# Kernel optimization log

Hardware: AMD Instinct MI355X
Metric: run time of the kernel (lower is better)

## Reference

```python
import jax, jax.numpy as jnp
import numpy as np

NEG_INF = -1e30
NUM_HEADS = 4
MEM_LEN = 16
RECURRENT_STEPS = 3
B, PLEN, GLEN, D = 16, 512, 16384, 256


def gated_attn(query, key, value, key_mask, Wq, Wk, Wv, Wo, Wg, bg):
    # GatedMultiHeadAttn.forward (pre/post lnorm off, add_zero_attn off, eval dropout)
    b, qlen, _ = query.shape
    klen = key.shape[1]
    hidden = Wq.shape[1]
    hd = hidden // NUM_HEADS
    hq = (query @ Wq).reshape(b, qlen, NUM_HEADS, hd)
    hk = (key @ Wk).reshape(b, klen, NUM_HEADS, hd)
    hv = (value @ Wv).reshape(b, klen, NUM_HEADS, hd)
    scale = 1.0 / np.sqrt(hd).astype(np.float32)
    score = jnp.einsum('bind,bjnd->bijn', hq, hk) * scale
    score = jnp.where((key_mask == 0)[:, None, :, None], NEG_INF, score)
    attn = jax.nn.softmax(score, axis=2)  # normalize over keys j
    vec = jnp.einsum('bijn,bjnd->bind', attn, hv).reshape(b, qlen, hidden)
    attn_out = vec @ Wo
    gate = jax.nn.sigmoid(jnp.concatenate([query, attn_out], axis=-1) @ Wg + bg)
    return gate * query + (1.0 - gate) * attn_out


def _attn_params(key, query_dim, kv_dim, hidden):
    ks = jax.random.split(key, 6)
    scale = 1.0 / np.sqrt(hidden // NUM_HEADS)
    Wq = jax.random.normal(ks[0], (query_dim, hidden), jnp.float32) * scale
    Wk = jax.random.normal(ks[1], (kv_dim, hidden), jnp.float32) * scale
    Wv = jax.random.normal(ks[2], (kv_dim, hidden), jnp.float32) * scale
    Wo = jax.random.normal(ks[3], (hidden, query_dim), jnp.float32) * scale
    Wg = jax.random.normal(ks[4], (2 * query_dim, query_dim), jnp.float32) * scale
    bg = jnp.ones((query_dim,), jnp.float32)
    return Wq, Wk, Wv, Wo, Wg, bg


def setup_inputs() -> dict:
    key = jax.random.key(0)
    ks = jax.random.split(key, 4)
    inp = {
        'pattern': jax.random.normal(ks[0], (B, PLEN, D), jnp.float32),
        'graph': jax.random.normal(ks[1], (B, GLEN, D), jnp.float32),
        'pattern_mask': jnp.ones((B, PLEN), jnp.int32),
        'graph_mask': jnp.ones((B, GLEN), jnp.int32),
    }
    p = _attn_params(ks[2], D, D, D)
    g = _attn_params(ks[3], D, D, D)
    for n, v in zip(['p_Wq', 'p_Wk', 'p_Wv', 'p_Wo', 'p_Wg', 'p_bg'], p):
        inp[n] = v
    for n, v in zip(['g_Wq', 'g_Wk', 'g_Wv', 'g_Wo', 'g_Wg', 'g_bg'], g):
        inp[n] = v
    return inp


def reference(pattern, graph, pattern_mask, graph_mask,
              p_Wq, p_Wk, p_Wv, p_Wo, p_Wg, p_bg,
              g_Wq, g_Wk, g_Wv, g_Wo, g_Wg, g_bg):
    b, glen, d = graph.shape
    stride = glen // MEM_LEN
    kernel = glen - (MEM_LEN - 1) * stride
    assert stride == kernel  # mem_len divides glen -> avg_pool1d == segment mean
    mem = graph.reshape(b, MEM_LEN, kernel, d).mean(axis=2)  # init_mem 'mean'
    mem_mask = graph_mask.reshape(b, MEM_LEN, kernel).max(axis=2)
    for _ in range(RECURRENT_STEPS):
        mem = gated_attn(mem, pattern, pattern, pattern_mask,
                         p_Wq, p_Wk, p_Wv, p_Wo, p_Wg, p_bg)
        mem = gated_attn(mem, graph, graph, graph_mask,
                         g_Wq, g_Wk, g_Wv, g_Wo, g_Wg, g_bg)
    return mem
```

## Files before the change

### kernel.cpp

```cpp
#include <hip/hip_runtime.h>
#include <stdint.h>

#define NH 4
#define HD 64
#define DM 256
#define BB 16
#define PLEN 512
#define GLEN 16384
#define ML 16
#define NCH_MAX 32

typedef __attribute__((ext_vector_type(8))) short bf16x8;
typedef __attribute__((ext_vector_type(4))) short s16x4;
typedef __attribute__((ext_vector_type(4))) float f32x4;
struct fl4 { float x, y, z, w; };

#define MFMA16(a, b, c) __builtin_amdgcn_mfma_f32_16x16x32_bf16((a), (b), (c), 0, 0, 0)

__device__ __forceinline__ float bf2f(short x) {
  union { unsigned u; float f; } v;
  v.u = ((unsigned)(unsigned short)x) << 16;
  return v.f;
}
__device__ __forceinline__ short f2bf(float x) {
  union { float f; unsigned u; } v;
  v.f = x;
  unsigned u = v.u;
  u += 0x7fffu + ((u >> 16) & 1u);
  return (short)(u >> 16);
}

__global__ void detect_dtype(const short* __restrict__ pattern, int* __restrict__ flag) {
  int t = threadIdx.x;
  int bad = 0;
  for (int i = t; i < 4096; i += 256) {
    float v = bf2f(pattern[2 * i]);
    if (!(fabsf(v) < 1e10f)) bad++;
  }
  __shared__ int cnt;
  if (t == 0) cnt = 0;
  __syncthreads();
  if (bad) atomicAdd(&cnt, bad);
  __syncthreads();
  if (t == 0) flag[0] = (cnt > 8) ? 1 : 0;
}

__global__ __launch_bounds__(512, 4) void proj_kv_fused(
    const void* __restrict__ Xraw, const short* __restrict__ WkT,
    const short* __restrict__ WvT, short* __restrict__ Kout,
    short* __restrict__ Vt, int L, float* __restrict__ partials,
    const int* __restrict__ flag) {
  __shared__ __align__(16) short Xs[64 * DM];
  __shared__ float scr[16 * DM];
  const int isf = flag[0];
  const int t = threadIdx.x;
  const int row0 = blockIdx.x * 64;
  const int tc2 = t & 31, tr2 = t >> 5;
  float s[8];
#pragma unroll
  for (int j = 0; j < 8; j++) s[j] = 0.f;
  if (isf) {
    const float* xf = (const float*)Xraw + (size_t)row0 * DM + tc2 * 8;
#pragma unroll
    for (int it = 0; it < 4; it++) {
      int row = it * 16 + tr2;
      fl4 v0 = *(const fl4*)(xf + (size_t)row * DM);
      fl4 v1 = *(const fl4*)(xf + (size_t)row * DM + 4);
      s[0] += v0.x; s[1] += v0.y; s[2] += v0.z; s[3] += v0.w;
      s[4] += v1.x; s[5] += v1.y; s[6] += v1.z; s[7] += v1.w;
      bf16x8 o;
      o[0] = f2bf(v0.x); o[1] = f2bf(v0.y); o[2] = f2bf(v0.z); o[3] = f2bf(v0.w);
      o[4] = f2bf(v1.x); o[5] = f2bf(v1.y); o[6] = f2bf(v1.z); o[7] = f2bf(v1.w);
      *(bf16x8*)(Xs + row * DM + (tc2 ^ (row & 7)) * 8) = o;
    }
  } else {
    const short* xb = (const short*)Xraw + (size_t)row0 * DM + tc2 * 8;
#pragma unroll
    for (int it = 0; it < 4; it++) {
      int row = it * 16 + tr2;
      bf16x8 v = *(const bf16x8*)(xb + (size_t)row * DM);
#pragma unroll
      for (int j = 0; j < 8; j++) s[j] += bf2f(v[j]);
      *(bf16x8*)(Xs + row * DM + (tc2 ^ (row & 7)) * 8) = v;
    }
  }
  if (partials) {
#pragma unroll
    for (int j = 0; j < 8; j++) scr[tr2 * DM + tc2 * 8 + j] = s[j];
  }
  __syncthreads();
  if (partials && t < DM) {
    float a = 0.f;
#pragma unroll
    for (int i = 0; i < 16; i++) a += scr[i * DM + t];
    partials[(size_t)blockIdx.x * DM + t] = a;
  }
  const int wave = t >> 6, lane = t & 63, quad = lane >> 4, l16 = lane & 15;
  const int kv = wave >> 2;
  const int wc = (wave & 3) * 64;
  const short* WT = kv ? WvT : WkT;
  f32x4 z = {0.f, 0.f, 0.f, 0.f};
  f32x4 acc[4][4];
#pragma unroll
  for (int i = 0; i < 4; i++)
#pragma unroll
    for (int j = 0; j < 4; j++) acc[i][j] = z;
#pragma unroll
  for (int kk = 0; kk < 8; kk++) {
    bf16x8 a[4], bw[4];
#pragma unroll
    for (int rt = 0; rt < 4; rt++) {
      int rw = rt * 16 + l16;
      a[rt] = *(const bf16x8*)(Xs + rw * DM + (((kk * 4 + quad) ^ (rw & 7)) * 8));
    }
#pragma unroll
    for (int ct = 0; ct < 4; ct++)
      bw[ct] = *(const bf16x8*)(WT + (size_t)(wc + ct * 16 + l16) * DM + kk * 32 + quad * 8);
#pragma unroll
    for (int rt = 0; rt < 4; rt++)
#pragma unroll
      for (int ct = 0; ct < 4; ct++)
        acc[rt][ct] = MFMA16(a[rt], bw[ct], acc[rt][ct]);
  }
  if (kv == 0) {
#pragma unroll
    for (int rt = 0; rt < 4; rt++)
#pragma unroll
      for (int ct = 0; ct < 4; ct++) {
        int col = wc + ct * 16 + l16;
#pragma unroll
        for (int r = 0; r < 4; r++)
          Kout[(size_t)(row0 + rt * 16 + quad * 4 + r) * DM + col] = f2bf(acc[rt][ct][r]);
      }
  } else {
    int bb = row0 / L, j0v = row0 % L;
#pragma unroll
    for (int rt = 0; rt < 4; rt++) {
      int j = j0v + rt * 16 + quad * 4;
#pragma unroll
      for (int ct = 0; ct < 4; ct++) {
        int c = wc + ct * 16 + l16;
        s16x4 pv;
#pragma unroll
        for (int r = 0; r < 4; r++) pv[r] = f2bf(acc[rt][ct][r]);
        *(s16x4*)(Vt + ((size_t)bb * DM + c) * L + j) = pv;
      }
    }
  }
}

__global__ __launch_bounds__(256) void finalize_q0(
    const float* __restrict__ partials, const void* __restrict__ Wq,
    float* __restrict__ mem, short* __restrict__ hq, const int* __restrict__ flag) {
  int b = blockIdx.x >> 4, m = blockIdx.x & 15;
  int t = threadIdx.x;
  int isf = flag[0];
  int p0 = b * 256 + m * 16;
  float s = 0.f;
#pragma unroll
  for (int i = 0; i < 16; i++) s += partials[(size_t)(p0 + i) * 256 + t];
  float v = s * (1.0f / 1024.0f);
  __shared__ float memrow[256];
  memrow[t] = bf2f(f2bf(v));
  mem[((size_t)b * ML + m) * DM + t] = v;
  __syncthreads();
  float acc = 0.f;
  if (isf) {
    const float* wf = (const float*)Wq;
    for (int k = 0; k < 256; k++)
      acc += memrow[k] * bf2f(f2bf(wf[(size_t)k * 256 + t]));
  } else {
    const short* wsp = (const short*)Wq;
    for (int k = 0; k < 256; k++)
      acc += memrow[k] * bf2f(wsp[(size_t)k * 256 + t]);
  }
  hq[((size_t)b * ML + m) * DM + t] = f2bf(acc);
}

struct WTArgs {
  const void* src[10];
  short* dst[10];
  int rows[10];
};

__global__ void transpose_w(WTArgs a, const int* __restrict__ flag) {
  int mid = blockIdx.z;
  int K = a.rows[mid];
  int tk = blockIdx.x, tn = blockIdx.y;
  if (tk * 32 >= K) return;
  int isf = flag[0];
  __shared__ short tile[32][33];
  const short* src = (const short*)a.src[mid];
  const float* srcf = (const float*)a.src[mid];
  short* dst = a.dst[mid];
  int tx = threadIdx.x, ty = threadIdx.y;
  for (int i = 0; i < 32; i += 8) {
    size_t idx = (size_t)(tk * 32 + ty + i) * 256 + tn * 32 + tx;
    tile[ty + i][tx] = isf ? f2bf(srcf[idx]) : src[idx];
  }
  __syncthreads();
  for (int i = 0; i < 32; i += 8)
    dst[(size_t)(tn * 32 + ty + i) * K + tk * 32 + tx] = tile[tx][ty + i];
}

__global__ void conv_bias(const void* p_bg, const void* g_bg, short* out,
                          const int* __restrict__ flag) {
  int t = threadIdx.x;
  int isf = flag[0];
  out[t] = isf ? f2bf(((const float*)p_bg)[t]) : ((const short*)p_bg)[t];
  out[256 + t] = isf ? f2bf(((const float*)g_bg)[t]) : ((const short*)g_bg)[t];
}

__global__ __launch_bounds__(256, 4) void flash_partial(
    const short* __restrict__ hq, const short* __restrict__ Kb,
    const short* __restrict__ Vt, const int* __restrict__ mask,
    float* __restrict__ pm, float* __restrict__ pl, float* __restrict__ pO,
    int L, int NCH) {
  int ch = blockIdx.x, b = blockIdx.y;
  int C = L / NCH;
  int t = threadIdx.x, wave = t >> 6, lane = t & 63, quad = lane >> 4, l16 = lane & 15;
  __shared__ __align__(16) short Plds[4][512];
  short* myP = &Plds[wave][0];
  const short* qbase = hq + ((size_t)b * ML + l16) * DM + wave * HD;
  bf16x8 aq0 = *(const bf16x8*)(qbase + quad * 8);
  bf16x8 aq1 = *(const bf16x8*)(qbase + 32 + quad * 8);
  f32x4 z = {0.f, 0.f, 0.f, 0.f};
  float m_run[4], l_run[4];
  f32x4 O[4];
#pragma unroll
  for (int r = 0; r < 4; r++) { m_run[r] = -1e30f; l_run[r] = 0.f; }
#pragma unroll
  for (int d = 0; d < 4; d++) O[d] = z;
  int j0 = ch * C;
  const float L2E = 1.44269504f;
  for (int jt = 0; jt < C; jt += 32) {
    f32x4 S[2];
#pragma unroll
    for (int tt = 0; tt < 2; tt++) {
      int j = j0 + jt + tt * 16 + l16;
      const short* kb = Kb + ((size_t)b * L + j) * DM + wave * HD;
      bf16x8 b0 = *(const bf16x8*)(kb + quad * 8);
      bf16x8 b1 = *(const bf16x8*)(kb + 32 + quad * 8);
      f32x4 s = MFMA16(aq0, b0, z);
      s = MFMA16(aq1, b1, s);
      int mk = mask[(size_t)b * L + j];
#pragma unroll
      for (int r = 0; r < 4; r++)
        S[tt][r] = mk ? s[r] * 0.125f : -1e30f;
    }
    float p[2][4], alpha[4];
#pragma unroll
    for (int r = 0; r < 4; r++) {
      float v = fmaxf(S[0][r], S[1][r]);
      v = fmaxf(v, __shfl_xor(v, 1, 16));
      v = fmaxf(v, __shfl_xor(v, 2, 16));
      v = fmaxf(v, __shfl_xor(v, 4, 16));
      v = fmaxf(v, __shfl_xor(v, 8, 16));
      float nm = fmaxf(m_run[r], v);
      alpha[r] = exp2f((m_run[r] - nm) * L2E);
      m_run[r] = nm;
      p[0][r] = exp2f((S[0][r] - nm) * L2E);
      p[1][r] = exp2f((S[1][r] - nm) * L2E);
      float ps = p[0][r] + p[1][r];
      ps += __shfl_xor(ps, 1, 16);
      ps += __shfl_xor(ps, 2, 16);
      ps += __shfl_xor(ps, 4, 16);
      ps += __shfl_xor(ps, 8, 16);
      l_run[r] = l_run[r] * alpha[r] + ps;
    }
#pragma unroll
    for (int d = 0; d < 4; d++)
#pragma unroll
      for (int r = 0; r < 4; r++) O[d][r] *= alpha[r];
#pragma unroll
    for (int tt = 0; tt < 2; tt++)
#pragma unroll
      for (int r = 0; r < 4; r++)
        myP[(quad * 4 + r) * 32 + tt * 16 + l16] = f2bf(p[tt][r]);
    __syncthreads();
    bf16x8 ap = *(const bf16x8*)(myP + l16 * 32 + quad * 8);
#pragma unroll
    for (int d = 0; d < 4; d++) {
      const short* vb = Vt + ((size_t)b * DM + wave * HD + d * 16 + l16) * L + j0 + jt + quad * 8;
      bf16x8 bv = *(const bf16x8*)vb;
      O[d] = MFMA16(ap, bv, O[d]);
    }
    __syncthreads();
  }
  size_t base = (((size_t)b * NCH + ch) * NH + wave) * ML;
  if (l16 == 0) {
#pragma unroll
    for (int r = 0; r < 4; r++) {
      pm[base + quad * 4 + r] = m_run[r];
      pl[base + quad * 4 + r] = l_run[r];
    }
  }
#pragma unroll
  for (int d = 0; d < 4; d++)
#pragma unroll
    for (int r = 0; r < 4; r++)
      pO[(base + quad * 4 + r) * 64 + d * 16 + l16] = O[d][r];
}

__global__ __launch_bounds__(256, 2) void epilogue(
    const float* __restrict__ pm, const float* __restrict__ pl,
    const float* __restrict__ pO, int NCH,
    float* __restrict__ mem, const short* __restrict__ WoT,
    const short* __restrict__ WgT, const short* __restrict__ bg,
    const short* __restrict__ WqT, short* __restrict__ hq,
    void* __restrict__ outb, const int* __restrict__ flag) {
  int b = blockIdx.x, t = threadIdx.x;
  int isf = flag[0];
  __shared__ float w_lds[NCH_MAX * 64];
  __shared__ float invL[64];
  __shared__ __align__(16) short vec_bf[ML * DM];
  __shared__ __align__(16) short mem_bf[ML * DM];
  __shared__ __align__(16) short attn_bf[ML * DM];
  __shared__ float attn_f[ML * DM];
  __shared__ __align__(16) short memn_bf[ML * DM];

  for (int idx = t; idx < ML * DM; idx += 256)
    mem_bf[idx] = f2bf(mem[(size_t)b * ML * DM + idx]);
  if (t < 64) {
    size_t base = (size_t)b * NCH * NH * ML + t;
    float M = -1e30f;
    for (int ch = 0; ch < NCH; ch++)
      M = fmaxf(M, pm[base + (size_t)ch * NH * ML]);
    float Ls = 0.f;
    for (int ch = 0; ch < NCH; ch++) {
      float w = exp2f((pm[base + (size_t)ch * NH * ML] - M) * 1.44269504f);
      w_lds[ch * 64 + t] = w;
      Ls += w * pl[base + (size_t)ch * NH * ML];
    }
    invL[t] = 1.0f / Ls;
  }
  __syncthreads();
  {
    int n = t >> 6, d = t & 63;
    for (int i = 0; i < 16; i++) {
      size_t pb = ((size_t)b * NCH * NH * ML + n * ML + i) * 64 + d;
      float o = 0.f;
      for (int ch = 0; ch < NCH; ch++)
        o += w_lds[ch * 64 + n * 16 + i] * pO[pb + (size_t)ch * NH * ML * 64];
      vec_bf[i * DM + n * 64 + d] = f2bf(o * invL[n * 16 + i]);
    }
  }
  __syncthreads();
  int wave = t >> 6, lane = t & 63, quad = lane >> 4, l16 = lane & 15;
  f32x4 z = {0.f, 0.f, 0.f, 0.f};
  f32x4 acc[4];
#pragma unroll
  for (int c = 0; c < 4; c++) acc[c] = z;
#pragma unroll
  for (int kk = 0; kk < 8; kk++) {
    bf16x8 a = *(const bf16x8*)(vec_bf + l16 * DM + kk * 32 + quad * 8);
#pragma unroll
    for (int ct = 0; ct < 4; ct++) {
      const short* wb = WoT + (size_t)(wave * 64 + ct * 16 + l16) * DM + kk * 32 + quad * 8;
      acc[ct] = MFMA16(a, *(const bf16x8*)wb, acc[ct]);
    }
  }
#pragma unroll
  for (int ct = 0; ct < 4; ct++)
#pragma unroll
    for (int r = 0; r < 4; r++) {
      int row = quad * 4 + r, col = wave * 64 + ct * 16 + l16;
      attn_f[row * DM + col] = acc[ct][r];
      attn_bf[row * DM + col] = f2bf(acc[ct][r]);
    }
  __syncthreads();
  f32x4 g[4];
#pragma unroll
  for (int c = 0; c < 4; c++) g[c] = z;
#pragma unroll
  for (int kk = 0; kk < 16; kk++) {
    bf16x8 a = (kk < 8)
        ? *(const bf16x8*)(mem_bf + l16 * DM + kk * 32 + quad * 8)
        : *(const bf16x8*)(attn_bf + l16 * DM + (kk - 8) * 32 + quad * 8);
#pragma unroll
    for (int ct = 0; ct < 4; ct++) {
      const short* wb = WgT + (size_t)(wave * 64 + ct * 16 + l16) * 512 + kk * 32 + quad * 8;
      g[ct] = MFMA16(a, *(const bf16x8*)wb, g[ct]);
    }
  }
#pragma unroll
  for (int ct = 0; ct < 4; ct++)
#pragma unroll
    for (int r = 0; r < 4; r++) {
      int row = quad * 4 + r, col = wave * 64 + ct * 16 + l16;
      float x = g[ct][r] + bf2f(bg[col]);
      float gg = 1.0f / (1.0f + exp2f(-x * 1.44269504f));
      float old = mem[(size_t)b * ML * DM + row * DM + col];
      float mn = gg * old + (1.0f - gg) * attn_f[row * DM + col];
      mem[(size_t)b * ML * DM + row * DM + col] = mn;
      memn_bf[row * DM + col] = f2bf(mn);
      if (outb) {
        size_t oi = (size_t)b * ML * DM + row * DM + col;
        if (isf) ((float*)outb)[oi] = mn;
        else ((short*)outb)[oi] = f2bf(mn);
      }
    }
  __syncthreads();
  if (WqT) {
    f32x4 h[4];
#pragma unroll
    for (int c = 0; c < 4; c++) h[c] = z;
#pragma unroll
    for (int kk = 0; kk < 8; kk++) {
      bf16x8 a = *(const bf16x8*)(memn_bf + l16 * DM + kk * 32 + quad * 8);
#pragma unroll
      for (int ct = 0; ct < 4; ct++) {
        const short* wb = WqT + (size_t)(wave * 64 + ct * 16 + l16) * DM + kk * 32 + quad * 8;
        h[ct] = MFMA16(a, *(const bf16x8*)wb, h[ct]);
      }
    }
#pragma unroll
    for (int ct = 0; ct < 4; ct++)
#pragma unroll
      for (int r = 0; r < 4; r++)
        hq[(size_t)b * ML * DM + (quad * 4 + r) * DM + wave * 64 + ct * 16 + l16] = f2bf(h[ct][r]);
  }
}

extern "C" void kernel_launch(void* const* d_in, const int* in_sizes, int n_in,
                              void* d_out, int out_size, void* d_ws, size_t ws_size,
                              hipStream_t stream) {
  const void* pattern = d_in[0];
  const void* graph = d_in[1];
  const int* pmask = (const int*)d_in[2];
  const int* gmask = (const int*)d_in[3];

  char* ws = (char*)d_ws;
  size_t off = 0;
  auto alloc = [&](size_t bytes) {
    void* p = ws + off;
    off = (off + bytes + 255) & ~(size_t)255;
    return p;
  };
  int* flag = (int*)alloc(4);
  int rows[10] = {256, 256, 256, 256, 512, 256, 256, 256, 256, 512};
  int srcidx[10] = {4, 5, 6, 7, 8, 10, 11, 12, 13, 14};
  short* WT[10];
  for (int i = 0; i < 10; i++) WT[i] = (short*)alloc((size_t)rows[i] * 256 * 2);
  short* bgc = (short*)alloc(512 * 2);
  short* Kp = (short*)alloc((size_t)BB * PLEN * DM * 2);
  short* Vpt = (short*)alloc((size_t)BB * PLEN * DM * 2);
  short* Kg = (short*)alloc((size_t)BB * GLEN * DM * 2);
  short* Vgt = (short*)alloc((size_t)BB * GLEN * DM * 2);
  short* hq = (short*)alloc((size_t)BB * ML * DM * 2);
  float* memf = (float*)alloc((size_t)BB * ML * DM * 4);
  float* pm = (float*)alloc((size_t)BB * NCH_MAX * NH * ML * 4);
  float* pl = (float*)alloc((size_t)BB * NCH_MAX * NH * ML * 4);
  float* pO = (float*)alloc((size_t)BB * NCH_MAX * NH * ML * 64 * 4);
  float* partG = (float*)alloc((size_t)(BB * GLEN / 64) * 256 * 4);
  if (off > ws_size) return;

  detect_dtype<<<dim3(1), dim3(256), 0, stream>>>((const short*)pattern, flag);

  WTArgs wa;
  for (int i = 0; i < 10; i++) {
    wa.src[i] = d_in[srcidx[i]];
    wa.dst[i] = WT[i];
    wa.rows[i] = rows[i];
  }
  transpose_w<<<dim3(16, 8, 10), dim3(32, 8), 0, stream>>>(wa, flag);
  conv_bias<<<dim3(1), dim3(256), 0, stream>>>(d_in[9], d_in[15], bgc, flag);

  proj_kv_fused<<<dim3(BB * GLEN / 64), dim3(512), 0, stream>>>(
      graph, WT[6], WT[7], Kg, Vgt, GLEN, partG, flag);
  proj_kv_fused<<<dim3(BB * PLEN / 64), dim3(512), 0, stream>>>(
      pattern, WT[1], WT[2], Kp, Vpt, PLEN, (float*)nullptr, flag);
  finalize_q0<<<dim3(BB * ML), dim3(256), 0, stream>>>(partG, d_in[4], memf, hq, flag);

  for (int s = 0; s < 3; s++) {
    flash_partial<<<dim3(8, BB), dim3(256), 0, stream>>>(hq, Kp, Vpt, pmask, pm, pl, pO, PLEN, 8);
    epilogue<<<dim3(BB), dim3(256), 0, stream>>>(pm, pl, pO, 8, memf, WT[3], WT[4], bgc,
                                                 (const short*)WT[5], hq, (void*)nullptr, flag);
    bool last = (s == 2);
    flash_partial<<<dim3(32, BB), dim3(256), 0, stream>>>(hq, Kg, Vgt, gmask, pm, pl, pO, GLEN, 32);
    epilogue<<<dim3(BB), dim3(256), 0, stream>>>(pm, pl, pO, 32, memf, WT[8], WT[9], bgc + 256,
                                                 last ? (const short*)nullptr : (const short*)WT[0],
                                                 hq, last ? d_out : (void*)nullptr, flag);
  }
}
```

Measured before the change: 1.109 ms.

## Transpose flash-partial score layout, drop block syncs, and raise chunk counts

The flash_partial kernel now computes scores with keys as the MFMA row operand and queries as columns. Each lane then holds one query's scores, so the running max and sum become per-lane scalars reduced with two cross-quad shuffles, and the mask loads as a single int4. Block-wide __syncthreads around the per-wave P staging are replaced by wave barriers plus an LDS waitcnt, and the P buffer gets padded rows. Chunk counts rise to 16 for pattern and 64 for graph to give more blocks, with the epilogue templated on the chunk count so its merge loops unroll; the cost is more partial results to write and combine.

```diff
diff --git a/kernel.cpp b/kernel.cpp
--- a/kernel.cpp
+++ b/kernel.cpp
@@ -8,7 +8,7 @@
 #define PLEN 512
 #define GLEN 16384
 #define ML 16
-#define NCH_MAX 32
+#define NCH_MAX 64
 
 typedef __attribute__((ext_vector_type(8))) short bf16x8;
 typedef __attribute__((ext_vector_type(4))) short s16x4;
@@ -219,81 +219,85 @@
   int ch = blockIdx.x, b = blockIdx.y;
   int C = L / NCH;
   int t = threadIdx.x, wave = t >> 6, lane = t & 63, quad = lane >> 4, l16 = lane & 15;
-  __shared__ __align__(16) short Plds[4][512];
+  __shared__ __align__(16) short Plds[4][16 * 40];
   short* myP = &Plds[wave][0];
   const short* qbase = hq + ((size_t)b * ML + l16) * DM + wave * HD;
-  bf16x8 aq0 = *(const bf16x8*)(qbase + quad * 8);
-  bf16x8 aq1 = *(const bf16x8*)(qbase + 32 + quad * 8);
+  bf16x8 bq0 = *(const bf16x8*)(qbase + quad * 8);
+  bf16x8 bq1 = *(const bf16x8*)(qbase + 32 + quad * 8);
   f32x4 z = {0.f, 0.f, 0.f, 0.f};
-  float m_run[4], l_run[4];
+  float m_run = -1e30f, l_run = 0.f;
   f32x4 O[4];
-#pragma unroll
-  for (int r = 0; r < 4; r++) { m_run[r] = -1e30f; l_run[r] = 0.f; }
 #pragma unroll
   for (int d = 0; d < 4; d++) O[d] = z;
   int j0 = ch * C;
   const float L2E = 1.44269504f;
+  const int* mrow = mask + (size_t)b * L + j0;
+  const short* k0 = Kb + ((size_t)b * L + j0 + l16) * DM + wave * HD + quad * 8;
+  const short* vbase = Vt + ((size_t)b * DM + wave * HD + l16) * L + j0 + quad * 8;
+  const size_t vstep = (size_t)16 * L;
   for (int jt = 0; jt < C; jt += 32) {
     f32x4 S[2];
 #pragma unroll
     for (int tt = 0; tt < 2; tt++) {
-      int j = j0 + jt + tt * 16 + l16;
-      const short* kb = Kb + ((size_t)b * L + j) * DM + wave * HD;
-      bf16x8 b0 = *(const bf16x8*)(kb + quad * 8);
-      bf16x8 b1 = *(const bf16x8*)(kb + 32 + quad * 8);
-      f32x4 s = MFMA16(aq0, b0, z);
-      s = MFMA16(aq1, b1, s);
-      int mk = mask[(size_t)b * L + j];
-#pragma unroll
-      for (int r = 0; r < 4; r++)
-        S[tt][r] = mk ? s[r] * 0.125f : -1e30f;
-    }
-    float p[2][4], alpha[4];
-#pragma unroll
-    for (int r = 0; r < 4; r++) {
-      float v = fmaxf(S[0][r], S[1][r]);
-      v = fmaxf(v, __shfl_xor(v, 1, 16));
-      v = fmaxf(v, __shfl_xor(v, 2, 16));
-      v = fmaxf(v, __shfl_xor(v, 4, 16));
-      v = fmaxf(v, __shfl_xor(v, 8, 16));
-      float nm = fmaxf(m_run[r], v);
-      alpha[r] = exp2f((m_run[r] - nm) * L2E);
-      m_run[r] = nm;
-      p[0][r] = exp2f((S[0][r] - nm) * L2E);
-      p[1][r] = exp2f((S[1][r] - nm) * L2E);
-      float ps = p[0][r] + p[1][r];
-      ps += __shfl_xor(ps, 1, 16);
-      ps += __shfl_xor(ps, 2, 16);
-      ps += __shfl_xor(ps, 4, 16);
-      ps += __shfl_xor(ps, 8, 16);
-      l_run[r] = l_run[r] * alpha[r] + ps;
-    }
+      const short* kb = k0 + (size_t)(jt + tt * 16) * DM;
+      bf16x8 a0 = *(const bf16x8*)kb;
+      bf16x8 a1 = *(const bf16x8*)(kb + 32);
+      f32x4 s = MFMA16(a0, bq0, z);
+      s = MFMA16(a1, bq1, s);
+      int4 mk = *(const int4*)(mrow + jt + tt * 16 + quad * 4);
+      S[tt][0] = mk.x ? s[0] * 0.125f : -1e30f;
+      S[tt][1] = mk.y ? s[1] * 0.125f : -1e30f;
+      S[tt][2] = mk.z ? s[2] * 0.125f : -1e30f;
+      S[tt][3] = mk.w ? s[3] * 0.125f : -1e30f;
+    }
+    float v = fmaxf(fmaxf(fmaxf(S[0][0], S[0][1]), fmaxf(S[0][2], S[0][3])),
+                    fmaxf(fmaxf(S[1][0], S[1][1]), fmaxf(S[1][2], S[1][3])));
+    v = fmaxf(v, __shfl_xor(v, 16, 64));
+    v = fmaxf(v, __shfl_xor(v, 32, 64));
+    float nm = fmaxf(m_run, v);
+    float alpha = exp2f((m_run - nm) * L2E);
+    m_run = nm;
+    float p[2][4];
+    float ps = 0.f;
+#pragma unroll
+    for (int tt = 0; tt < 2; tt++)
+#pragma unroll
+      for (int r = 0; r < 4; r++) {
+        p[tt][r] = exp2f((S[tt][r] - nm) * L2E);
+        ps += p[tt][r];
+      }
+    ps += __shfl_xor(ps, 16, 64);
+    ps += __shfl_xor(ps, 32, 64);
+    l_run = l_run * alpha + ps;
+    float alr[4];
+#pragma unroll
+    for (int r = 0; r < 4; r++) alr[r] = __shfl(alpha, quad * 4 + r, 64);
 #pragma unroll
     for (int d = 0; d < 4; d++)
 #pragma unroll
-      for (int r = 0; r < 4; r++) O[d][r] *= alpha[r];
-#pragma unroll
-    for (int tt = 0; tt < 2; tt++)
-#pragma unroll
-      for (int r = 0; r < 4; r++)
-        myP[(quad * 4 + r) * 32 + tt * 16 + l16] = f2bf(p[tt][r]);
-    __syncthreads();
-    bf16x8 ap = *(const bf16x8*)(myP + l16 * 32 + quad * 8);
+      for (int r = 0; r < 4; r++) O[d][r] *= alr[r];
+#pragma unroll
+    for (int tt = 0; tt < 2; tt++) {
+      s16x4 pk;
+#pragma unroll
+      for (int r = 0; r < 4; r++) pk[r] = f2bf(p[tt][r]);
+      *(s16x4*)(myP + l16 * 40 + tt * 16 + quad * 4) = pk;
+    }
+    __builtin_amdgcn_wave_barrier();
+    __builtin_amdgcn_s_waitcnt(0xc07f);
+    __builtin_amdgcn_wave_barrier();
+    bf16x8 ap = *(const bf16x8*)(myP + l16 * 40 + quad * 8);
+    const short* vb = vbase + jt;
 #pragma unroll
     for (int d = 0; d < 4; d++) {
-      const short* vb = Vt + ((size_t)b * DM + wave * HD + d * 16 + l16) * L + j0 + jt + quad * 8;
-      bf16x8 bv = *(const bf16x8*)vb;
+      bf16x8 bv = *(const bf16x8*)(vb + (size_t)d * vstep);
       O[d] = MFMA16(ap, bv, O[d]);
     }
-    __syncthreads();
   }
   size_t base = (((size_t)b * NCH + ch) * NH + wave) * ML;
-  if (l16 == 0) {
-#pragma unroll
-    for (int r = 0; r < 4; r++) {
-      pm[base + quad * 4 + r] = m_run[r];
-      pl[base + quad * 4 + r] = l_run[r];
-    }
+  if (lane < 16) {
+    pm[base + l16] = m_run;
+    pl[base + l16] = l_run;
   }
 #pragma unroll
   for (int d = 0; d < 4; d++)
@@ -302,16 +306,17 @@
       pO[(base + quad * 4 + r) * 64 + d * 16 + l16] = O[d][r];
 }
 
+template <int NCH>
 __global__ __launch_bounds__(256, 2) void epilogue(
     const float* __restrict__ pm, const float* __restrict__ pl,
-    const float* __restrict__ pO, int NCH,
+    const float* __restrict__ pO,
     float* __restrict__ mem, const short* __restrict__ WoT,
     const short* __restrict__ WgT, const short* __restrict__ bg,
     const short* __restrict__ WqT, short* __restrict__ hq,
     void* __restrict__ outb, const int* __restrict__ flag) {
   int b = blockIdx.x, t = threadIdx.x;
   int isf = flag[0];
-  __shared__ float w_lds[NCH_MAX * 64];
+  __shared__ float w_lds[NCH * 64];
   __shared__ float invL[64];
   __shared__ __align__(16) short vec_bf[ML * DM];
   __shared__ __align__(16) short mem_bf[ML * DM];
@@ -324,9 +329,11 @@
   if (t < 64) {
     size_t base = (size_t)b * NCH * NH * ML + t;
     float M = -1e30f;
+#pragma unroll
     for (int ch = 0; ch < NCH; ch++)
       M = fmaxf(M, pm[base + (size_t)ch * NH * ML]);
     float Ls = 0.f;
+#pragma unroll
     for (int ch = 0; ch < NCH; ch++) {
       float w = exp2f((pm[base + (size_t)ch * NH * ML] - M) * 1.44269504f);
       w_lds[ch * 64 + t] = w;
@@ -340,6 +347,7 @@
     for (int i = 0; i < 16; i++) {
       size_t pb = ((size_t)b * NCH * NH * ML + n * ML + i) * 64 + d;
       float o = 0.f;
+#pragma unroll
       for (int ch = 0; ch < NCH; ch++)
         o += w_lds[ch * 64 + n * 16 + i] * pO[pb + (size_t)ch * NH * ML * 64];
       vec_bf[i * DM + n * 64 + d] = f2bf(o * invL[n * 16 + i]);
@@ -472,14 +480,15 @@
       pattern, WT[1], WT[2], Kp, Vpt, PLEN, (float*)nullptr, flag);
   finalize_q0<<<dim3(BB * ML), dim3(256), 0, stream>>>(partG, d_in[4], memf, hq, flag);
 
+  const int NCHP = 16, NCHG = 64;
   for (int s = 0; s < 3; s++) {
-    flash_partial<<<dim3(8, BB), dim3(256), 0, stream>>>(hq, Kp, Vpt, pmask, pm, pl, pO, PLEN, 8);
-    epilogue<<<dim3(BB), dim3(256), 0, stream>>>(pm, pl, pO, 8, memf, WT[3], WT[4], bgc,
-                                                 (const short*)WT[5], hq, (void*)nullptr, flag);
+    flash_partial<<<dim3(NCHP, BB), dim3(256), 0, stream>>>(hq, Kp, Vpt, pmask, pm, pl, pO, PLEN, NCHP);
+    epilogue<NCHP><<<dim3(BB), dim3(256), 0, stream>>>(pm, pl, pO, memf, WT[3], WT[4], bgc,
+                                                       (const short*)WT[5], hq, (void*)nullptr, flag);
     bool last = (s == 2);
-    flash_partial<<<dim3(32, BB), dim3(256), 0, stream>>>(hq, Kg, Vgt, gmask, pm, pl, pO, GLEN, 32);
-    epilogue<<<dim3(BB), dim3(256), 0, stream>>>(pm, pl, pO, 32, memf, WT[8], WT[9], bgc + 256,
-                                                 last ? (const short*)nullptr : (const short*)WT[0],
-                                                 hq, last ? d_out : (void*)nullptr, flag);
-  }
-}
+    flash_partial<<<dim3(NCHG, BB), dim3(256), 0, stream>>>(hq, Kg, Vgt, gmask, pm, pl, pO, GLEN, NCHG);
+    epilogue<NCHG><<<dim3(BB), dim3(256), 0, stream>>>(pm, pl, pO, memf, WT[8], WT[9], bgc + 256,
+                                                       last ? (const short*)nullptr : (const short*)WT[0],
+                                                       hq, last ? d_out : (void*)nullptr, flag);
+  }
+}
```

Result: slower. 1.600 ms (+44.3%).

## Make K/V projection persistent over multiple tiles with double-buffered prefetch

Applied to the files above, without the earlier changes.

Each projection block now processes four 64-row tiles using double-buffered shared memory. The next tile's fp32 loads are issued and converted to bf16 while the current tile's MFMAs run, so global latency hides behind compute. The segment column sums are now reduced directly with atomicAdd into a per-segment buffer that is zeroed by a memset, which removes the large partials array and the 16-way reduction in finalize. In exchange, the colsum re-reads the input tile from global memory, the kernel uses more registers, and the grid holds fewer blocks.

```diff
diff --git a/kernel.cpp b/kernel.cpp
--- a/kernel.cpp
+++ b/kernel.cpp
@@ -9,6 +9,7 @@
 #define GLEN 16384
 #define ML 16
 #define NCH_MAX 32
+#define PT 4
 
 typedef __attribute__((ext_vector_type(8))) short bf16x8;
 typedef __attribute__((ext_vector_type(4))) short s16x4;
@@ -50,100 +51,131 @@
     const short* __restrict__ WvT, short* __restrict__ Kout,
     short* __restrict__ Vt, int L, float* __restrict__ partials,
     const int* __restrict__ flag) {
-  __shared__ __align__(16) short Xs[64 * DM];
-  __shared__ float scr[16 * DM];
+  __shared__ __align__(16) short Xs[2][64 * DM];
   const int isf = flag[0];
   const int t = threadIdx.x;
-  const int row0 = blockIdx.x * 64;
   const int tc2 = t & 31, tr2 = t >> 5;
-  float s[8];
-#pragma unroll
-  for (int j = 0; j < 8; j++) s[j] = 0.f;
-  if (isf) {
-    const float* xf = (const float*)Xraw + (size_t)row0 * DM + tc2 * 8;
-#pragma unroll
-    for (int it = 0; it < 4; it++) {
-      int row = it * 16 + tr2;
-      fl4 v0 = *(const fl4*)(xf + (size_t)row * DM);
-      fl4 v1 = *(const fl4*)(xf + (size_t)row * DM + 4);
-      s[0] += v0.x; s[1] += v0.y; s[2] += v0.z; s[3] += v0.w;
-      s[4] += v1.x; s[5] += v1.y; s[6] += v1.z; s[7] += v1.w;
-      bf16x8 o;
-      o[0] = f2bf(v0.x); o[1] = f2bf(v0.y); o[2] = f2bf(v0.z); o[3] = f2bf(v0.w);
-      o[4] = f2bf(v1.x); o[5] = f2bf(v1.y); o[6] = f2bf(v1.z); o[7] = f2bf(v1.w);
-      *(bf16x8*)(Xs + row * DM + (tc2 ^ (row & 7)) * 8) = o;
-    }
-  } else {
-    const short* xb = (const short*)Xraw + (size_t)row0 * DM + tc2 * 8;
-#pragma unroll
-    for (int it = 0; it < 4; it++) {
-      int row = it * 16 + tr2;
-      bf16x8 v = *(const bf16x8*)(xb + (size_t)row * DM);
-#pragma unroll
-      for (int j = 0; j < 8; j++) s[j] += bf2f(v[j]);
-      *(bf16x8*)(Xs + row * DM + (tc2 ^ (row & 7)) * 8) = v;
-    }
-  }
-  if (partials) {
-#pragma unroll
-    for (int j = 0; j < 8; j++) scr[tr2 * DM + tc2 * 8 + j] = s[j];
-  }
-  __syncthreads();
-  if (partials && t < DM) {
-    float a = 0.f;
-#pragma unroll
-    for (int i = 0; i < 16; i++) a += scr[i * DM + t];
-    partials[(size_t)blockIdx.x * DM + t] = a;
-  }
   const int wave = t >> 6, lane = t & 63, quad = lane >> 4, l16 = lane & 15;
   const int kv = wave >> 2;
   const int wc = (wave & 3) * 64;
   const short* WT = kv ? WvT : WkT;
-  f32x4 z = {0.f, 0.f, 0.f, 0.f};
-  f32x4 acc[4][4];
-#pragma unroll
-  for (int i = 0; i < 4; i++)
-#pragma unroll
-    for (int j = 0; j < 4; j++) acc[i][j] = z;
-#pragma unroll
-  for (int kk = 0; kk < 8; kk++) {
-    bf16x8 a[4], bw[4];
-#pragma unroll
-    for (int rt = 0; rt < 4; rt++) {
-      int rw = rt * 16 + l16;
-      a[rt] = *(const bf16x8*)(Xs + rw * DM + (((kk * 4 + quad) ^ (rw & 7)) * 8));
-    }
-#pragma unroll
-    for (int ct = 0; ct < 4; ct++)
-      bw[ct] = *(const bf16x8*)(WT + (size_t)(wc + ct * 16 + l16) * DM + kk * 32 + quad * 8);
-#pragma unroll
-    for (int rt = 0; rt < 4; rt++)
-#pragma unroll
-      for (int ct = 0; ct < 4; ct++)
-        acc[rt][ct] = MFMA16(a[rt], bw[ct], acc[rt][ct]);
-  }
-  if (kv == 0) {
-#pragma unroll
-    for (int rt = 0; rt < 4; rt++)
-#pragma unroll
-      for (int ct = 0; ct < 4; ct++) {
-        int col = wc + ct * 16 + l16;
-#pragma unroll
-        for (int r = 0; r < 4; r++)
-          Kout[(size_t)(row0 + rt * 16 + quad * 4 + r) * DM + col] = f2bf(acc[rt][ct][r]);
+  const int tile0 = blockIdx.x * PT;
+
+  fl4 Rf[8];
+  bf16x8 Rb[4];
+
+  auto ISSUE = [&](int tile) {
+    const float* xf = (const float*)Xraw + (size_t)tile * (64 * DM) + tc2 * 8;
+#pragma unroll
+    for (int it = 0; it < 4; it++) {
+      size_t ro = (size_t)(it * 16 + tr2) * DM;
+      Rf[it * 2] = *(const fl4*)(xf + ro);
+      Rf[it * 2 + 1] = *(const fl4*)(xf + ro + 4);
+    }
+  };
+  auto CVTREG = [&]() {
+#pragma unroll
+    for (int it = 0; it < 4; it++) {
+      fl4 v0 = Rf[it * 2], v1 = Rf[it * 2 + 1];
+      bf16x8 o;
+      o[0] = f2bf(v0.x); o[1] = f2bf(v0.y); o[2] = f2bf(v0.z); o[3] = f2bf(v0.w);
+      o[4] = f2bf(v1.x); o[5] = f2bf(v1.y); o[6] = f2bf(v1.z); o[7] = f2bf(v1.w);
+      Rb[it] = o;
+    }
+  };
+  auto WRITE = [&](int buf) {
+    short* xs = &Xs[buf][0];
+#pragma unroll
+    for (int it = 0; it < 4; it++) {
+      int row = it * 16 + tr2;
+      *(bf16x8*)(xs + row * DM + (tc2 ^ (row & 7)) * 8) = Rb[it];
+    }
+  };
+  auto STAGE_BF16 = [&](int tile, int buf) {
+    const short* xb = (const short*)Xraw + (size_t)tile * (64 * DM) + tc2 * 8;
+    short* xs = &Xs[buf][0];
+#pragma unroll
+    for (int it = 0; it < 4; it++) {
+      int row = it * 16 + tr2;
+      bf16x8 v = *(const bf16x8*)(xb + (size_t)row * DM);
+      *(bf16x8*)(xs + row * DM + (tc2 ^ (row & 7)) * 8) = v;
+    }
+  };
+  auto COLSUM = [&](int tile) {
+    if (partials == nullptr || t >= DM) return;
+    int seg = (tile * 64) >> 10;
+    float s = 0.f;
+    if (isf) {
+      const float* xf = (const float*)Xraw + (size_t)tile * (64 * DM) + t;
+#pragma unroll 8
+      for (int r = 0; r < 64; r++) s += xf[(size_t)r * DM];
+    } else {
+      const short* xb = (const short*)Xraw + (size_t)tile * (64 * DM) + t;
+#pragma unroll 8
+      for (int r = 0; r < 64; r++) s += bf2f(xb[(size_t)r * DM]);
+    }
+    atomicAdd(partials + (size_t)seg * DM + t, s);
+  };
+
+  if (isf) { ISSUE(tile0); CVTREG(); }
+#pragma unroll 2
+  for (int tt = 0; tt < PT; tt++) {
+    const int tile = tile0 + tt, buf = tt & 1;
+    if (isf) WRITE(buf); else STAGE_BF16(tile, buf);
+    __syncthreads();
+    if (isf && tt + 1 < PT) ISSUE(tile + 1);
+    COLSUM(tile);
+    f32x4 z4 = {0.f, 0.f, 0.f, 0.f};
+    f32x4 acc[4][4];
+#pragma unroll
+    for (int i = 0; i < 4; i++)
+#pragma unroll
+      for (int j = 0; j < 4; j++) acc[i][j] = z4;
+    const short* xs = &Xs[buf][0];
+#pragma unroll
+    for (int kh = 0; kh < 2; kh++) {
+#pragma unroll
+      for (int k2 = 0; k2 < 4; k2++) {
+        const int kk = kh * 4 + k2;
+        bf16x8 bw[4];
+#pragma unroll
+        for (int ct = 0; ct < 4; ct++)
+          bw[ct] = *(const bf16x8*)(WT + (size_t)(wc + ct * 16 + l16) * DM + kk * 32 + quad * 8);
+#pragma unroll
+        for (int rt = 0; rt < 4; rt++) {
+          int rw = rt * 16 + l16;
+          bf16x8 a = *(const bf16x8*)(xs + rw * DM + (((kk * 4 + quad) ^ (rw & 7)) * 8));
+#pragma unroll
+          for (int ct = 0; ct < 4; ct++)
+            acc[rt][ct] = MFMA16(a, bw[ct], acc[rt][ct]);
+        }
       }
-  } else {
-    int bb = row0 / L, j0v = row0 % L;
-#pragma unroll
-    for (int rt = 0; rt < 4; rt++) {
-      int j = j0v + rt * 16 + quad * 4;
-#pragma unroll
-      for (int ct = 0; ct < 4; ct++) {
-        int c = wc + ct * 16 + l16;
-        s16x4 pv;
-#pragma unroll
-        for (int r = 0; r < 4; r++) pv[r] = f2bf(acc[rt][ct][r]);
-        *(s16x4*)(Vt + ((size_t)bb * DM + c) * L + j) = pv;
+      if (kh == 0 && isf && tt + 1 < PT) CVTREG();
+    }
+    const int row0 = tile * 64;
+    if (kv == 0) {
+#pragma unroll
+      for (int rt = 0; rt < 4; rt++)
+#pragma unroll
+        for (int ct = 0; ct < 4; ct++) {
+          int col = wc + ct * 16 + l16;
+#pragma unroll
+          for (int r = 0; r < 4; r++)
+            Kout[(size_t)(row0 + rt * 16 + quad * 4 + r) * DM + col] = f2bf(acc[rt][ct][r]);
+        }
+    } else {
+      int bb = row0 / L, j0v = row0 % L;
+#pragma unroll
+      for (int rt = 0; rt < 4; rt++) {
+        int j = j0v + rt * 16 + quad * 4;
+#pragma unroll
+        for (int ct = 0; ct < 4; ct++) {
+          int c = wc + ct * 16 + l16;
+          s16x4 pv;
+#pragma unroll
+          for (int r = 0; r < 4; r++) pv[r] = f2bf(acc[rt][ct][r]);
+          *(s16x4*)(Vt + ((size_t)bb * DM + c) * L + j) = pv;
+        }
       }
     }
   }
@@ -155,10 +187,7 @@
   int b = blockIdx.x >> 4, m = blockIdx.x & 15;
   int t = threadIdx.x;
   int isf = flag[0];
-  int p0 = b * 256 + m * 16;
-  float s = 0.f;
-#pragma unroll
-  for (int i = 0; i < 16; i++) s += partials[(size_t)(p0 + i) * 256 + t];
+  float s = partials[((size_t)b * ML + m) * DM + t];
   float v = s * (1.0f / 1024.0f);
   __shared__ float memrow[256];
   memrow[t] = bf2f(f2bf(v));
@@ -452,7 +481,7 @@
   float* pm = (float*)alloc((size_t)BB * NCH_MAX * NH * ML * 4);
   float* pl = (float*)alloc((size_t)BB * NCH_MAX * NH * ML * 4);
   float* pO = (float*)alloc((size_t)BB * NCH_MAX * NH * ML * 64 * 4);
-  float* partG = (float*)alloc((size_t)(BB * GLEN / 64) * 256 * 4);
+  float* partG = (float*)alloc((size_t)BB * ML * DM * 4);
   if (off > ws_size) return;
 
   detect_dtype<<<dim3(1), dim3(256), 0, stream>>>((const short*)pattern, flag);
@@ -466,9 +495,10 @@
   transpose_w<<<dim3(16, 8, 10), dim3(32, 8), 0, stream>>>(wa, flag);
   conv_bias<<<dim3(1), dim3(256), 0, stream>>>(d_in[9], d_in[15], bgc, flag);
 
-  proj_kv_fused<<<dim3(BB * GLEN / 64), dim3(512), 0, stream>>>(
+  hipMemsetAsync(partG, 0, (size_t)BB * ML * DM * 4, stream);
+  proj_kv_fused<<<dim3(BB * GLEN / 64 / PT), dim3(512), 0, stream>>>(
       graph, WT[6], WT[7], Kg, Vgt, GLEN, partG, flag);
-  proj_kv_fused<<<dim3(BB * PLEN / 64), dim3(512), 0, stream>>>(
+  proj_kv_fused<<<dim3(BB * PLEN / 64 / PT), dim3(512), 0, stream>>>(
       pattern, WT[1], WT[2], Kp, Vpt, PLEN, (float*)nullptr, flag);
   finalize_q0<<<dim3(BB * ML), dim3(256), 0, stream>>>(partG, d_in[4], memf, hq, flag);
 
```

Result: slower. 1.709 ms (+54.2%).

## Make K/V projection persistent with double-buffered async global-to-LDS tile loads

Applied to the files above, without the earlier changes.

The graph K/V projection kernel becomes persistent: each block handles 16 tiles of 32 rows, using global_load_lds to prefetch the next raw tile into a second LDS buffer while computing on the current one. The fp32-to-bf16 conversion now happens when operands are read from LDS rather than at staging, and per-segment column sums for the memory initialisation are accumulated across tiles, so finalize only adds two partials. This aims to hide HBM latency for the large graph read. In exchange it halves the row tile per MFMA pass, doubles LDS per block (64 KB), and relies on hand-written vmcnt waits and barriers.

```diff
diff --git a/kernel.cpp b/kernel.cpp
--- a/kernel.cpp
+++ b/kernel.cpp
@@ -9,11 +9,13 @@
 #define GLEN 16384
 #define ML 16
 #define NCH_MAX 32
+#define TROWS 32
+#define TBYTES_F32 32768
+#define TBYTES_BF16 16384
 
 typedef __attribute__((ext_vector_type(8))) short bf16x8;
 typedef __attribute__((ext_vector_type(4))) short s16x4;
 typedef __attribute__((ext_vector_type(4))) float f32x4;
-struct fl4 { float x, y, z, w; };
 
 #define MFMA16(a, b, c) __builtin_amdgcn_mfma_f32_16x16x32_bf16((a), (b), (c), 0, 0, 0)
 
@@ -29,6 +31,12 @@
   u += 0x7fffu + ((u >> 16) & 1u);
   return (short)(u >> 16);
 }
+__device__ __forceinline__ bf16x8 pack8(f32x4 a, f32x4 b) {
+  bf16x8 o;
+  o[0] = f2bf(a[0]); o[1] = f2bf(a[1]); o[2] = f2bf(a[2]); o[3] = f2bf(a[3]);
+  o[4] = f2bf(b[0]); o[5] = f2bf(b[1]); o[6] = f2bf(b[2]); o[7] = f2bf(b[3]);
+  return o;
+}
 
 __global__ void detect_dtype(const short* __restrict__ pattern, int* __restrict__ flag) {
   int t = threadIdx.x;
@@ -45,107 +53,162 @@
   if (t == 0) flag[0] = (cnt > 8) ? 1 : 0;
 }
 
+__device__ __forceinline__ void stage_tile(const void* Xraw, int isf, int tile,
+                                           char* lds, int wave, int lane) {
+  if (isf) {
+    const char* gb = (const char*)Xraw + (size_t)tile * TBYTES_F32;
+#pragma unroll
+    for (int k = 0; k < 4; k++) {
+      int row = k * 8 + wave;
+      const char* src = gb + row * 1024 + ((lane ^ (row & 7)) * 16);
+      char* dst = lds + k * 8192 + wave * 1024;
+      __builtin_amdgcn_global_load_lds(
+          (const __attribute__((address_space(1))) unsigned int*)src,
+          (__attribute__((address_space(3))) unsigned int*)dst, 16, 0, 0);
+    }
+  } else {
+    const char* gb = (const char*)Xraw + (size_t)tile * TBYTES_BF16;
+#pragma unroll
+    for (int k = 0; k < 2; k++) {
+      int row = k * 16 + wave * 2 + (lane >> 5);
+      const char* src = gb + row * 512 + (((lane & 31) ^ (row & 7)) * 16);
+      char* dst = lds + k * 8192 + wave * 1024;
+      __builtin_amdgcn_global_load_lds(
+          (const __attribute__((address_space(1))) unsigned int*)src,
+          (__attribute__((address_space(3))) unsigned int*)dst, 16, 0, 0);
+    }
+  }
+}
+
 __global__ __launch_bounds__(512, 4) void proj_kv_fused(
     const void* __restrict__ Xraw, const short* __restrict__ WkT,
     const short* __restrict__ WvT, short* __restrict__ Kout,
     short* __restrict__ Vt, int L, float* __restrict__ partials,
-    const int* __restrict__ flag) {
-  __shared__ __align__(16) short Xs[64 * DM];
-  __shared__ float scr[16 * DM];
+    const int* __restrict__ flag, int PTr) {
+  __shared__ __align__(16) char Xb[2][TBYTES_F32];
   const int isf = flag[0];
   const int t = threadIdx.x;
-  const int row0 = blockIdx.x * 64;
-  const int tc2 = t & 31, tr2 = t >> 5;
-  float s[8];
-#pragma unroll
-  for (int j = 0; j < 8; j++) s[j] = 0.f;
-  if (isf) {
-    const float* xf = (const float*)Xraw + (size_t)row0 * DM + tc2 * 8;
-#pragma unroll
-    for (int it = 0; it < 4; it++) {
-      int row = it * 16 + tr2;
-      fl4 v0 = *(const fl4*)(xf + (size_t)row * DM);
-      fl4 v1 = *(const fl4*)(xf + (size_t)row * DM + 4);
-      s[0] += v0.x; s[1] += v0.y; s[2] += v0.z; s[3] += v0.w;
-      s[4] += v1.x; s[5] += v1.y; s[6] += v1.z; s[7] += v1.w;
-      bf16x8 o;
-      o[0] = f2bf(v0.x); o[1] = f2bf(v0.y); o[2] = f2bf(v0.z); o[3] = f2bf(v0.w);
-      o[4] = f2bf(v1.x); o[5] = f2bf(v1.y); o[6] = f2bf(v1.z); o[7] = f2bf(v1.w);
-      *(bf16x8*)(Xs + row * DM + (tc2 ^ (row & 7)) * 8) = o;
-    }
-  } else {
-    const short* xb = (const short*)Xraw + (size_t)row0 * DM + tc2 * 8;
-#pragma unroll
-    for (int it = 0; it < 4; it++) {
-      int row = it * 16 + tr2;
-      bf16x8 v = *(const bf16x8*)(xb + (size_t)row * DM);
-#pragma unroll
-      for (int j = 0; j < 8; j++) s[j] += bf2f(v[j]);
-      *(bf16x8*)(Xs + row * DM + (tc2 ^ (row & 7)) * 8) = v;
-    }
-  }
+  const int wave = t >> 6, lane = t & 63, quad = lane >> 4, l16 = lane & 15;
+  const int kv = wave >> 2, wc = (wave & 3) * 64;
+  const short* WT = kv ? WvT : WkT;
+  const int tile0 = blockIdx.x * PTr;
+  const int crow0 = (t >> 8) * 16, ccol = t & 255;
+  float csum = 0.f;
+
+  stage_tile(Xraw, isf, tile0, &Xb[0][0], wave, lane);
+
+  for (int j = 0; j < PTr; j++) {
+    const int tile = tile0 + j;
+    const int buf = j & 1;
+    if (j + 1 < PTr) {
+      stage_tile(Xraw, isf, tile + 1, &Xb[buf ^ 1][0], wave, lane);
+      if (isf) asm volatile("s_waitcnt vmcnt(4)" ::: "memory");
+      else     asm volatile("s_waitcnt vmcnt(2)" ::: "memory");
+    } else {
+      asm volatile("s_waitcnt vmcnt(0)" ::: "memory");
+    }
+    __builtin_amdgcn_s_barrier();
+
+    int lz = 0;
+    asm volatile("" : "+v"(lz));
+    const short* WTj = WT + lz;
+
+    const char* xb = &Xb[buf][0];
+    f32x4 z4 = {0.f, 0.f, 0.f, 0.f};
+    f32x4 acc[2][4];
+#pragma unroll
+    for (int i = 0; i < 2; i++)
+#pragma unroll
+      for (int c = 0; c < 4; c++) acc[i][c] = z4;
+
+    if (isf) {
+#pragma unroll
+      for (int kk = 0; kk < 8; kk++) {
+        bf16x8 bw[4];
+#pragma unroll
+        for (int ct = 0; ct < 4; ct++)
+          bw[ct] = *(const bf16x8*)(WTj + (size_t)(wc + ct * 16 + l16) * DM + kk * 32 + quad * 8);
+        const int g0 = kk * 8 + quad * 2;
+#pragma unroll
+        for (int rt = 0; rt < 2; rt++) {
+          int rw = rt * 16 + l16, f = rw & 7;
+          f32x4 x0 = *(const f32x4*)(xb + rw * 1024 + ((g0 ^ f) * 16));
+          f32x4 x1 = *(const f32x4*)(xb + rw * 1024 + (((g0 + 1) ^ f) * 16));
+          bf16x8 a = pack8(x0, x1);
+#pragma unroll
+          for (int ct = 0; ct < 4; ct++) acc[rt][ct] = MFMA16(a, bw[ct], acc[rt][ct]);
+        }
+      }
+    } else {
+#pragma unroll
+      for (int kk = 0; kk < 8; kk++) {
+        bf16x8 bw[4];
+#pragma unroll
+        for (int ct = 0; ct < 4; ct++)
+          bw[ct] = *(const bf16x8*)(WTj + (size_t)(wc + ct * 16 + l16) * DM + kk * 32 + quad * 8);
+        const int g = kk * 4 + quad;
+#pragma unroll
+        for (int rt = 0; rt < 2; rt++) {
+          int rw = rt * 16 + l16;
+          bf16x8 a = *(const bf16x8*)(xb + rw * 512 + ((g ^ (rw & 7)) * 16));
+#pragma unroll
+          for (int ct = 0; ct < 4; ct++) acc[rt][ct] = MFMA16(a, bw[ct], acc[rt][ct]);
+        }
+      }
+    }
+
+    if (partials) {
+      if (isf) {
+#pragma unroll
+        for (int i = 0; i < 16; i++) {
+          int r = crow0 + i;
+          csum += *(const float*)(xb + r * 1024 + (((ccol >> 2) ^ (r & 7)) * 16) + (ccol & 3) * 4);
+        }
+      } else {
+#pragma unroll
+        for (int i = 0; i < 16; i++) {
+          int r = crow0 + i;
+          csum += bf2f(*(const short*)(xb + r * 512 + (((ccol >> 3) ^ (r & 7)) * 16) + (ccol & 7) * 2));
+        }
+      }
+    }
+
+    const int row0 = tile * TROWS;
+    if (kv == 0) {
+#pragma unroll
+      for (int rt = 0; rt < 2; rt++)
+#pragma unroll
+        for (int ct = 0; ct < 4; ct++) {
+          int col = wc + ct * 16 + l16;
+#pragma unroll
+          for (int r = 0; r < 4; r++)
+            Kout[(size_t)(row0 + rt * 16 + quad * 4 + r) * DM + col] = f2bf(acc[rt][ct][r]);
+        }
+    } else {
+      int bb = row0 / L, j0v = row0 % L;
+#pragma unroll
+      for (int rt = 0; rt < 2; rt++) {
+        int jj = j0v + rt * 16 + quad * 4;
+#pragma unroll
+        for (int ct = 0; ct < 4; ct++) {
+          int c = wc + ct * 16 + l16;
+          s16x4 pv;
+#pragma unroll
+          for (int r = 0; r < 4; r++) pv[r] = f2bf(acc[rt][ct][r]);
+          *(s16x4*)(Vt + ((size_t)bb * DM + c) * L + jj) = pv;
+        }
+      }
+    }
+
+    asm volatile("" ::: "memory");
+    __builtin_amdgcn_s_barrier();
+  }
+
   if (partials) {
-#pragma unroll
-    for (int j = 0; j < 8; j++) scr[tr2 * DM + tc2 * 8 + j] = s[j];
-  }
-  __syncthreads();
-  if (partials && t < DM) {
-    float a = 0.f;
-#pragma unroll
-    for (int i = 0; i < 16; i++) a += scr[i * DM + t];
-    partials[(size_t)blockIdx.x * DM + t] = a;
-  }
-  const int wave = t >> 6, lane = t & 63, quad = lane >> 4, l16 = lane & 15;
-  const int kv = wave >> 2;
-  const int wc = (wave & 3) * 64;
-  const short* WT = kv ? WvT : WkT;
-  f32x4 z = {0.f, 0.f, 0.f, 0.f};
-  f32x4 acc[4][4];
-#pragma unroll
-  for (int i = 0; i < 4; i++)
-#pragma unroll
-    for (int j = 0; j < 4; j++) acc[i][j] = z;
-#pragma unroll
-  for (int kk = 0; kk < 8; kk++) {
-    bf16x8 a[4], bw[4];
-#pragma unroll
-    for (int rt = 0; rt < 4; rt++) {
-      int rw = rt * 16 + l16;
-      a[rt] = *(const bf16x8*)(Xs + rw * DM + (((kk * 4 + quad) ^ (rw & 7)) * 8));
-    }
-#pragma unroll
-    for (int ct = 0; ct < 4; ct++)
-      bw[ct] = *(const bf16x8*)(WT + (size_t)(wc + ct * 16 + l16) * DM + kk * 32 + quad * 8);
-#pragma unroll
-    for (int rt = 0; rt < 4; rt++)
-#pragma unroll
-      for (int ct = 0; ct < 4; ct++)
-        acc[rt][ct] = MFMA16(a[rt], bw[ct], acc[rt][ct]);
-  }
-  if (kv == 0) {
-#pragma unroll
-    for (int rt = 0; rt < 4; rt++)
-#pragma unroll
-      for (int ct = 0; ct < 4; ct++) {
-        int col = wc + ct * 16 + l16;
-#pragma unroll
-        for (int r = 0; r < 4; r++)
-          Kout[(size_t)(row0 + rt * 16 + quad * 4 + r) * DM + col] = f2bf(acc[rt][ct][r]);
-      }
-  } else {
-    int bb = row0 / L, j0v = row0 % L;
-#pragma unroll
-    for (int rt = 0; rt < 4; rt++) {
-      int j = j0v + rt * 16 + quad * 4;
-#pragma unroll
-      for (int ct = 0; ct < 4; ct++) {
-        int c = wc + ct * 16 + l16;
-        s16x4 pv;
-#pragma unroll
-        for (int r = 0; r < 4; r++) pv[r] = f2bf(acc[rt][ct][r]);
-        *(s16x4*)(Vt + ((size_t)bb * DM + c) * L + j) = pv;
-      }
-    }
+    float* scrf = (float*)&Xb[0][0];
+    if (t >= 256) scrf[t - 256] = csum;
+    __syncthreads();
+    if (t < 256) partials[(size_t)blockIdx.x * 256 + t] = csum + scrf[t];
   }
 }
 
@@ -153,12 +216,10 @@
     const float* __restrict__ partials, const void* __restrict__ Wq,
     float* __restrict__ mem, short* __restrict__ hq, const int* __restrict__ flag) {
   int b = blockIdx.x >> 4, m = blockIdx.x & 15;
+  int seg = b * ML + m;
   int t = threadIdx.x;
   int isf = flag[0];
-  int p0 = b * 256 + m * 16;
-  float s = 0.f;
-#pragma unroll
-  for (int i = 0; i < 16; i++) s += partials[(size_t)(p0 + i) * 256 + t];
+  float s = partials[(size_t)(2 * seg) * 256 + t] + partials[(size_t)(2 * seg + 1) * 256 + t];
   float v = s * (1.0f / 1024.0f);
   __shared__ float memrow[256];
   memrow[t] = bf2f(f2bf(v));
@@ -452,7 +513,7 @@
   float* pm = (float*)alloc((size_t)BB * NCH_MAX * NH * ML * 4);
   float* pl = (float*)alloc((size_t)BB * NCH_MAX * NH * ML * 4);
   float* pO = (float*)alloc((size_t)BB * NCH_MAX * NH * ML * 64 * 4);
-  float* partG = (float*)alloc((size_t)(BB * GLEN / 64) * 256 * 4);
+  float* partG = (float*)alloc((size_t)512 * 256 * 4);
   if (off > ws_size) return;
 
   detect_dtype<<<dim3(1), dim3(256), 0, stream>>>((const short*)pattern, flag);
@@ -466,10 +527,10 @@
   transpose_w<<<dim3(16, 8, 10), dim3(32, 8), 0, stream>>>(wa, flag);
   conv_bias<<<dim3(1), dim3(256), 0, stream>>>(d_in[9], d_in[15], bgc, flag);
 
-  proj_kv_fused<<<dim3(BB * GLEN / 64), dim3(512), 0, stream>>>(
-      graph, WT[6], WT[7], Kg, Vgt, GLEN, partG, flag);
-  proj_kv_fused<<<dim3(BB * PLEN / 64), dim3(512), 0, stream>>>(
-      pattern, WT[1], WT[2], Kp, Vpt, PLEN, (float*)nullptr, flag);
+  proj_kv_fused<<<dim3(512), dim3(512), 0, stream>>>(
+      graph, WT[6], WT[7], Kg, Vgt, GLEN, partG, flag, 16);
+  proj_kv_fused<<<dim3(256), dim3(512), 0, stream>>>(
+      pattern, WT[1], WT[2], Kp, Vpt, PLEN, (float*)nullptr, flag, 1);
   finalize_q0<<<dim3(BB * ML), dim3(256), 0, stream>>>(partG, d_in[4], memf, hq, flag);
 
   for (int s = 0; s < 3; s++) {
```

Measured after the change: 1.237 ms. +11.6%, slower.
